# Kernel tuning notes

Hardware: AMD Instinct MI355X
Metric: run time of the kernel (lower is better)

Reference implementation:

```python
import jax, jax.numpy as jnp
import numpy as np

# 5x5 Gaussian-Laplacian template: kernel = (4*GL) * GL_T, with a2=-a1/8, a3=-a1/16
GL_T = np.zeros((5, 5), np.float32)
GL_T[2, 2] = 1.0
for r, c in [(1, 2), (2, 1), (2, 3), (3, 2)]:
    GL_T[r, c] = -1.0 / 8.0
for r, c in [(0, 2), (1, 1), (1, 3), (2, 0), (2, 4), (3, 1), (3, 3), (4, 2)]:
    GL_T[r, c] = -1.0 / 16.0

SOB0 = np.array([[1, 2, 1], [0, 0, 0], [-1, -2, -1]], np.float32)
SOB45 = np.array([[2, 1, 0], [1, 0, -1], [0, -1, -2]], np.float32)
SOB90 = np.array([[1, 0, -1], [2, 0, -2], [1, 0, -1]], np.float32)
SOB135 = np.array([[0, -1, -2], [1, 0, -1], [2, 1, 0]], np.float32)

# cubic-spaced threshold value table: (10-0)*(i/100)^3, i=0..100
X_VALUES = np.array([10.0 * (i / 100.0) ** 3 for i in range(101)], np.float32)


def conv2d(x, w, stride=1, padding=0):
    return jax.lax.conv_general_dilated(
        x, w, (stride, stride), ((padding, padding), (padding, padding)),
        dimension_numbers=("NCHW", "OIHW", "NCHW"))


def avg_pool(x, k, s, p):
    # PyTorch AvgPool2d default count_include_pad=True -> divide by k*k always
    s_ = jax.lax.reduce_window(x, 0.0, jax.lax.add, (1, 1, k, k), (1, 1, s, s),
                               ((0, 0), (0, 0), (p, p), (p, p)))
    return s_ / float(k * k)


def _gdm(x, gdm_weight, conv_w, bn_gamma, bn_beta, bn_mean, bn_var):
    x = avg_pool(x, 3, 2, 1)                                  # [B,3,H/2,W/2]
    image_a = jnp.mean(x, axis=1, keepdims=True)              # [B,1,h,w]
    y = conv2d(x, conv_w, stride=2, padding=3)                # ConvBN(3,5,7,s2)
    y = (y - bn_mean[None, :, None, None]) * jax.lax.rsqrt(bn_var + 1e-5)[None, :, None, None]
    y = y * bn_gamma[None, :, None, None] + bn_beta[None, :, None, None]
    weight_att = jnp.tanh(jnp.mean(y, axis=(2, 3)))           # [B,5]

    a1 = gdm_weight[0, 0] * 4.0
    kgl = (a1 * jnp.asarray(GL_T))[None, None]                # [1,1,5,5]
    x_GL = jnp.abs(conv2d(image_a, kgl, stride=1, padding=2))
    x_GL = jnp.where(x_GL < 1e-6, 0.0, x_GL)                  # abs/threshold; relu is no-op

    b, _, h, w = x_GL.shape
    x_t = x_GL.reshape(b, 1, -1)                              # [B,1,HW]
    x_max = jnp.max(x_t, axis=-1)                             # [B,1]
    pos = x_t > 0
    all_sum = jnp.sum(pos, axis=-1)                           # [B,1]
    xv = jnp.asarray(X_VALUES)[None, :, None]                 # [1,101,1]
    sub_sum = jnp.sum(pos & (x_t <= xv), axis=-1)             # [B,101]
    percentage = sub_sum / all_sum                            # [B,101] float

    params = jnp.stack([0.2 + 0.05 * weight_att[:, 1],
                        0.4 + 0.05 * weight_att[:, 2],
                        0.6 + 0.05 * weight_att[:, 3],
                        0.8 + 0.05 * weight_att[:, 4]])       # [4,B]
    thr_pct = jnp.sort(params, axis=0).T                      # [B,4]
    z = jnp.abs(percentage[:, None, :] - thr_pct[:, :, None]) # [B,4,101]
    closest = jnp.argmin(z, axis=-1)                          # [B,4]
    threshold = jnp.asarray(X_VALUES)[closest]                # [B,4]

    tmin = jnp.concatenate([jnp.zeros_like(x_max), threshold], axis=-1)[:, :, None]  # [B,5,1]
    tmax = jnp.concatenate([threshold, x_max], axis=-1)[:, :, None]                  # [B,5,1]
    mask = ((x_t > tmin) & (x_t <= tmax)).astype(jnp.float32)                        # [B,5,HW]
    m = mask.reshape(b, 5, h, w)

    m = avg_pool(m, 9, 1, 4)
    m = avg_pool(m, 9, 1, 4)
    m = avg_pool(m, 9, 2, 4)                                  # [B,5,h/2,w/2]
    mf = m.reshape(b, 5, -1)
    mn = jnp.min(mf, axis=2, keepdims=True)
    mx = jnp.max(mf, axis=2, keepdims=True)
    return ((mf - mn) / (mx - mn)).reshape(b, 5, h // 2, w // 2)


def _hge(feat, hge_weight, fc_w, fc_b):
    # directional kernels built from entries of the learned 3x3 weight
    Sob0 = hge_weight[:, :, 0, 0][:, :, None, None]
    Sob45 = hge_weight[:, :, 0, 1][:, :, None, None]
    Sob90 = hge_weight[:, :, 0, 2][:, :, None, None]
    Sob135 = hge_weight[:, :, 1, 0][:, :, None, None]
    a1 = (hge_weight[:, :, 2, 2] * 4.0)[:, :, None, None]
    x_0 = conv2d(feat, Sob0 * jnp.asarray(SOB0), 1, 1)
    x_45 = conv2d(feat, Sob45 * jnp.asarray(SOB45), 1, 1)
    x_90 = conv2d(feat, Sob90 * jnp.asarray(SOB90), 1, 1)
    x_135 = conv2d(feat, Sob135 * jnp.asarray(SOB135), 1, 1)
    x_GL = conv2d(feat, a1 * jnp.asarray(GL_T), 1, 2)
    x_out = jnp.concatenate([x_0, x_45, x_90, x_135, x_GL], axis=1)  # [B,5*C,H,W]
    return conv2d(x_out, fc_w) + fc_b[None, :, None, None]


def setup_inputs() -> dict:
    key = jax.random.key(0)
    ks = jax.random.split(key, 6)
    return {
        "x": jax.random.normal(ks[0], (8, 3, 512, 512), jnp.float32),
        "gdm_weight": jax.random.normal(ks[1], (1, 5), jnp.float32) * 0.5,
        "conv_w": jax.random.normal(ks[2], (5, 3, 7, 7), jnp.float32) * 0.05,
        "bn_gamma": jnp.ones((5,), jnp.float32),
        "bn_beta": jnp.zeros((5,), jnp.float32),
        "bn_mean": jnp.zeros((5,), jnp.float32),
        "bn_var": jnp.ones((5,), jnp.float32),
        "feat": jax.random.normal(ks[3], (8, 64, 128, 128), jnp.float32),
        "hge_weight": jax.random.normal(ks[4], (64, 64, 3, 3), jnp.float32) * 0.05,
        "fc_w": jax.random.normal(ks[5], (64, 320, 1, 1), jnp.float32) * 0.05,
        "fc_b": jnp.zeros((64,), jnp.float32),
    }


def reference(x, gdm_weight, conv_w, bn_gamma, bn_beta, bn_mean, bn_var,
              feat, hge_weight, fc_w, fc_b):
    gdm_out = _gdm(x, gdm_weight, conv_w, bn_gamma, bn_beta, bn_mean, bn_var)
    hge_out = _hge(feat, hge_weight, fc_w, fc_b)
    return gdm_out, hge_out
```

## Files before the change

### kernel.cpp

```cpp
#include <hip/hip_runtime.h>
#include <hip/hip_bf16.h>
#include <math.h>

#define WS_AT    0
#define WS_YSUM  20480
#define WS_XMAX  20520
#define WS_HIST  20528
#define WS_THR   21344
#define WS_MN    21376
#define WS_MX    21440
#define WS_XP    21504
#define WS_IA    1594368
#define WS_XGL   2118656

#define GDM_OUT  655360

static __device__ __forceinline__ float xv_val(int i) {
    double t = (double)i / 100.0;
    return (float)(10.0 * t * t * t);
}

__global__ __launch_bounds__(256) void k_front(const float* __restrict__ x,
                                               const float* __restrict__ hw,
                                               const float* __restrict__ fcw,
                                               float* __restrict__ xp,
                                               float* __restrict__ ia,
                                               float* __restrict__ At,
                                               float* __restrict__ zr) {
    int bid = blockIdx.x;
    if (bid < 2048) {
        int idx = bid * 256 + threadIdx.x;
        int b = idx >> 16; int p = idx & 65535; int oy = p >> 8; int ox = p & 255;
        float cs[3];
#pragma unroll
        for (int c = 0; c < 3; ++c) {
            const float* src = x + (((size_t)(b * 3 + c)) << 18);
            float s = 0.f;
#pragma unroll
            for (int dy = -1; dy <= 1; ++dy) {
                int iy = 2 * oy + dy; if ((unsigned)iy >= 512u) continue;
#pragma unroll
                for (int dx = -1; dx <= 1; ++dx) {
                    int ix = 2 * ox + dx; if ((unsigned)ix >= 512u) continue;
                    s += src[iy * 512 + ix];
                }
            }
            cs[c] = s * (1.f / 9.f);
            xp[(((size_t)(b * 3 + c)) << 16) + p] = cs[c];
        }
        ia[(((size_t)b) << 16) + p] = (cs[0] + cs[1] + cs[2]) * (1.f / 3.f);
    } else if (bid < 2128) {
        int idx = (bid - 2048) * 256 + threadIdx.x;
        int o = idx & 63; int k = idx >> 6;
        int d = k >> 6; int c = k & 63;
        const int goff[5] = {0, 1, 2, 3, 8};
        float s = 0.f;
        for (int m = 0; m < 64; ++m)
            s += fcw[o * 320 + d * 64 + m] * hw[(m * 64 + c) * 9 + goff[d]];
        At[k * 64 + o] = s * ((d == 4) ? 4.f : 1.f);
    } else {
#pragma unroll
        for (int q = 0; q < 4; ++q) {
            int i = threadIdx.x + 256 * q;
            if (i < 864) zr[i] = 0.f;
        }
    }
}

__global__ __launch_bounds__(256) void k_conv7(const float* __restrict__ xp,
                                               const float* __restrict__ w,
                                               float* __restrict__ ysum) {
    int b = blockIdx.y;
    int p = blockIdx.x * 256 + threadIdx.x;
    int oy = p >> 7, ox = p & 127;
    __shared__ float wsm[735];
    for (int l = threadIdx.x; l < 735; l += 256) wsm[l] = w[l];
    __syncthreads();
    float s[5] = {0.f, 0.f, 0.f, 0.f, 0.f};
    for (int ic = 0; ic < 3; ++ic) {
        const float* src = xp + (((size_t)(b * 3 + ic)) << 16);
#pragma unroll
        for (int r = 0; r < 7; ++r) {
            int iy = 2 * oy - 3 + r; if ((unsigned)iy >= 256u) continue;
#pragma unroll
            for (int ss = 0; ss < 7; ++ss) {
                int ix = 2 * ox - 3 + ss; if ((unsigned)ix >= 256u) continue;
                float v = src[iy * 256 + ix];
                int wi = (ic * 7 + r) * 7 + ss;
#pragma unroll
                for (int co = 0; co < 5; ++co) s[co] = fmaf(wsm[co * 147 + wi], v, s[co]);
            }
        }
    }
    __shared__ float red[256];
#pragma unroll
    for (int co = 0; co < 5; ++co) {
        red[threadIdx.x] = s[co]; __syncthreads();
        for (int off = 128; off > 0; off >>= 1) {
            if (threadIdx.x < off) red[threadIdx.x] += red[threadIdx.x + off];
            __syncthreads();
        }
        if (threadIdx.x == 0) atomicAdd(&ysum[b * 5 + co], red[0]);
        __syncthreads();
    }
}

__global__ __launch_bounds__(256) void k_gl_hist(const float* __restrict__ ia,
                                                 const float* __restrict__ gdmw,
                                                 float* __restrict__ xgl,
                                                 int* __restrict__ hist,
                                                 unsigned* __restrict__ xmax) {
    int b = blockIdx.y;
    int p = blockIdx.x * 256 + threadIdx.x;
    int y = p >> 8, x = p & 255;
    __shared__ float xv[101];
    __shared__ int sh[102];
    __shared__ float redm[256];
    if (threadIdx.x < 101) xv[threadIdx.x] = xv_val(threadIdx.x);
    if (threadIdx.x < 102) sh[threadIdx.x] = 0;
    __syncthreads();
    const float* src = ia + (((size_t)b) << 16);
    float a1 = gdmw[0] * 4.f;
    auto rd = [&](int dy, int dx) -> float {
        int iy = y + dy, ix = x + dx;
        if ((unsigned)iy >= 256u || (unsigned)ix >= 256u) return 0.f;
        return src[iy * 256 + ix];
    };
    float acc = rd(0, 0)
        - 0.125f  * (rd(-1, 0) + rd(0, -1) + rd(0, 1) + rd(1, 0))
        - 0.0625f * (rd(-2, 0) + rd(-1, -1) + rd(-1, 1) + rd(0, -2) +
                     rd(0, 2) + rd(1, -1) + rd(1, 1) + rd(2, 0));
    float raw = fabsf(a1 * acc);
    float val = (raw < 1e-6f) ? 0.f : raw;
    xgl[(((size_t)b) << 16) + p] = val;
    if (val > 0.f) {
        int lo = 0, hi = 101;
        while (lo < hi) { int mid = (lo + hi) >> 1; if (val <= xv[mid]) hi = mid; else lo = mid + 1; }
        atomicAdd(&sh[lo], 1);
    }
    redm[threadIdx.x] = val; __syncthreads();
    for (int off = 128; off > 0; off >>= 1) {
        if (threadIdx.x < off) redm[threadIdx.x] = fmaxf(redm[threadIdx.x], redm[threadIdx.x + off]);
        __syncthreads();
    }
    if (threadIdx.x == 0) atomicMax(&xmax[b], __float_as_uint(redm[0]));
    if (threadIdx.x < 102 && sh[threadIdx.x]) atomicAdd(&hist[b * 102 + threadIdx.x], sh[threadIdx.x]);
}

__global__ void k_thresholds(const float* __restrict__ ysum, const float* __restrict__ gamma,
                             const float* __restrict__ beta, const float* __restrict__ mean,
                             const float* __restrict__ var, const int* __restrict__ hist,
                             float* __restrict__ thr, unsigned* __restrict__ mnb,
                             unsigned* __restrict__ mxb) {
    int b = threadIdx.x;
    if (b >= 8) {
        if (b < 48) { mnb[b - 8] = 0x7f7fffffu; mxb[b - 8] = 0u; }
        return;
    }
    float wa[5];
    for (int c = 1; c < 5; ++c) {
        float m = ysum[b * 5 + c] * (1.f / 16384.f);
        wa[c] = tanhf((m - mean[c]) * rsqrtf(var[c] + 1e-5f) * gamma[c] + beta[c]);
    }
    float pr[4] = {0.2f + 0.05f * wa[1], 0.4f + 0.05f * wa[2],
                   0.6f + 0.05f * wa[3], 0.8f + 0.05f * wa[4]};
    auto sw = [&](int i, int j) { if (pr[i] > pr[j]) { float t = pr[i]; pr[i] = pr[j]; pr[j] = t; } };
    sw(0, 1); sw(2, 3); sw(0, 2); sw(1, 3); sw(1, 2);
    int all = 0;
    for (int i = 0; i <= 101; ++i) all += hist[b * 102 + i];
    float bestz[4] = {1e30f, 1e30f, 1e30f, 1e30f};
    int besti[4] = {0, 0, 0, 0};
    int cum = 0;
    for (int i = 0; i <= 100; ++i) {
        cum += hist[b * 102 + i];
        float pct = (float)cum / (float)all;
        for (int t = 0; t < 4; ++t) {
            float z = fabsf(pct - pr[t]);
            if (z < bestz[t]) { bestz[t] = z; besti[t] = i; }
        }
    }
    for (int t = 0; t < 4; ++t) thr[b * 4 + t] = xv_val(besti[t]);
}

#define F1_STR 268
__global__ __launch_bounds__(256) void k_hv1(const float* __restrict__ in,
                                             const float* __restrict__ thr,
                                             const unsigned* __restrict__ xmax,
                                             float* __restrict__ outp) {
    int plane = blockIdx.y;
    int r0 = blockIdx.x * 8;
    int b = plane / 5, band = plane - 5 * b;
    float tmin = (band == 0) ? 0.f : thr[b * 4 + band - 1];
    float tmax = (band == 4) ? __uint_as_float(xmax[b]) : thr[b * 4 + band];
    const float* src = in + (((size_t)b) << 16);
    __shared__ float mr[16][F1_STR];
    __shared__ float hh[16][256];
    int tid = threadIdx.x;
    for (int l = tid; l < 16 * 256; l += 256) {
        int i = l >> 8, c = l & 255;
        int rr = r0 - 4 + i;
        float v = ((unsigned)rr < 256u) ? src[rr * 256 + c] : 0.f;
        v = (v > tmin && v <= tmax) ? 1.f : 0.f;
        mr[i][c + 4] = v;
    }
    if (tid < 128) { int i = tid >> 3, p = tid & 7; mr[i][p < 4 ? p : 256 + p] = 0.f; }
    __syncthreads();
    {
        int r = tid >> 4, x0 = (tid & 15) * 16;
        float w[24];
#pragma unroll
        for (int k = 0; k < 6; ++k) {
            float4 q = *(const float4*)&mr[r][x0 + 4 * k];
            w[4 * k] = q.x; w[4 * k + 1] = q.y; w[4 * k + 2] = q.z; w[4 * k + 3] = q.w;
        }
        float o[16];
        float s = 0.f;
#pragma unroll
        for (int k = 0; k < 9; ++k) s += w[k];
#pragma unroll
        for (int j = 0; j < 16; ++j) {
            o[j] = s * (1.f / 9.f);
            if (j < 15) s += w[j + 9] - w[j];
        }
#pragma unroll
        for (int k = 0; k < 4; ++k) {
            float4 q = {o[4 * k], o[4 * k + 1], o[4 * k + 2], o[4 * k + 3]};
            *(float4*)&hh[r][x0 + 4 * k] = q;
        }
    }
    __syncthreads();
    {
        int c = tid;
        float ld[16];
#pragma unroll
        for (int i = 0; i < 16; ++i) ld[i] = hh[i][c];
        float s = 0.f;
#pragma unroll
        for (int k = 0; k < 9; ++k) s += ld[k];
        float* dst = outp + (((size_t)plane) << 16);
#pragma unroll
        for (int j = 0; j < 8; ++j) {
            dst[(r0 + j) * 256 + c] = s * (1.f / 9.f);
            if (j < 7) s += ld[j + 9] - ld[j];
        }
    }
}

__global__ __launch_bounds__(256) void k_hv2s2(const float* __restrict__ in,
                                               float* __restrict__ outp,
                                               unsigned* __restrict__ mnb,
                                               unsigned* __restrict__ mxb) {
    int plane = blockIdx.y;
    int r0 = blockIdx.x * 8;
    __shared__ float mr[31][264];
    __shared__ float hh[31][256];
    int tid = threadIdx.x;
    const float* src = in + (((size_t)plane) << 16);
    for (int l = tid; l < 31 * 264; l += 256) {
        int i = l / 264, c = l - i * 264;
        int rr = 2 * r0 - 8 + i, cc = c - 4;
        mr[i][c] = ((unsigned)rr < 256u && (unsigned)cc < 256u) ? src[rr * 256 + cc] : 0.f;
    }
    __syncthreads();
    for (int l = tid; l < 31 * 256; l += 256) {
        int i = l >> 8, x = l & 255;
        float s = 0.f;
#pragma unroll
        for (int k = 0; k < 9; ++k) s += mr[i][x + k];
        hh[i][x] = s * (1.f / 9.f);
    }
    __syncthreads();
    for (int l = tid; l < 23 * 256; l += 256) {
        int i2 = l >> 8, x = l & 255;
        float s = 0.f;
#pragma unroll
        for (int k = 0; k < 9; ++k) s += hh[i2 + k][x];
        float v = s * (1.f / 9.f);
        if ((unsigned)(2 * r0 - 4 + i2) >= 256u) v = 0.f;
        mr[i2][x + 4] = v;
    }
    if (tid < 184) { int i2 = tid / 8, p = tid & 7; mr[i2][p < 4 ? p : 256 + p] = 0.f; }
    __syncthreads();
    for (int l = tid; l < 23 * 128; l += 256) {
        int i2 = l >> 7, ox = l & 127;
        float s = 0.f;
#pragma unroll
        for (int k = 0; k < 9; ++k) s += mr[i2][2 * ox + k];
        hh[i2][ox] = s * (1.f / 9.f);
    }
    __syncthreads();
    float vmn = 1e30f, vmx = -1e30f;
    float* dst = outp + (size_t)plane * 16384;
#pragma unroll
    for (int q = 0; q < 4; ++q) {
        int l = tid + 256 * q;
        int jj = l >> 7, ox = l & 127;
        float s = 0.f;
#pragma unroll
        for (int k = 0; k < 9; ++k) s += hh[2 * jj + k][ox];
        s *= (1.f / 9.f);
        dst[(r0 + jj) * 128 + ox] = s;
        vmn = fminf(vmn, s); vmx = fmaxf(vmx, s);
    }
    __syncthreads();
    float* smn = &hh[23][0];
    float* smx = &hh[24][0];
    smn[tid] = vmn; smx[tid] = vmx; __syncthreads();
    for (int off = 128; off > 0; off >>= 1) {
        if (tid < off) {
            smn[tid] = fminf(smn[tid], smn[tid + off]);
            smx[tid] = fmaxf(smx[tid], smx[tid + off]);
        }
        __syncthreads();
    }
    if (tid == 0) {
        atomicMin(&mnb[plane], __float_as_uint(smn[0]));
        atomicMax(&mxb[plane], __float_as_uint(smx[0]));
    }
}

__global__ __launch_bounds__(256) void k_norm(const float* __restrict__ in,
                                              const unsigned* __restrict__ mnb,
                                              const unsigned* __restrict__ mxb,
                                              float* __restrict__ gdm) {
    int i4 = blockIdx.x * 256 + threadIdx.x;
    int idx = i4 * 4;
    int plane = idx >> 14;
    float mn = __uint_as_float(mnb[plane]), mx = __uint_as_float(mxb[plane]);
    float inv = 1.f / (mx - mn);
    float4 v = *(const float4*)&in[idx];
    float4 o = {(v.x - mn) * inv, (v.y - mn) * inv, (v.z - mn) * inv, (v.w - mn) * inv};
    *(float4*)&gdm[idx] = o;
}

__global__ __launch_bounds__(512, 2) void k_hge(const float* __restrict__ feat,
                                                const float* __restrict__ At,
                                                const float* __restrict__ fcb,
                                                float* __restrict__ out) {
    int tile = blockIdx.x, b = blockIdx.y;
    int ty = (tile >> 3) * 16, tx = (tile & 7) * 16;
    int tid = threadIdx.x;
    int grp = tid >> 8, tg = tid & 255;
    __shared__ float ft[2][20][21];
    __shared__ float tl[2][5][256];
    __shared__ float al[2][2][5][64];
    int og = tg >> 5, pg = tg & 31;
    float acc[8][4];
#pragma unroll
    for (int i = 0; i < 8; ++i)
#pragma unroll
        for (int j = 0; j < 4; ++j) acc[i][j] = 0.f;

    const float* cur[3];
    int str[3];
    bool ok[3];
#pragma unroll
    for (int j = 0; j < 3; ++j) {
        int l = tid + 512 * j;
        cur[j] = nullptr; str[j] = 0; ok[j] = false;
        if (l < 800) {
            int ch = (l >= 400); int rem = l - ch * 400;
            int r = rem / 20, cx = rem - r * 20;
            int gy = ty - 2 + r, gx = tx - 2 + cx;
            if ((unsigned)gy < 128u && (unsigned)gx < 128u) {
                cur[j] = feat + (((size_t)(b * 64 + ch)) << 14) + gy * 128 + gx;
                str[j] = 2 << 14;
                ok[j] = true;
            }
        } else if (l < 1440) {
            int q = l - 800;
            int ch = (q >= 320); int k = q - ch * 320;
            cur[j] = At + (k >> 6) * 4096 + ch * 64 + (k & 63);
            str[j] = 128;
            ok[j] = true;
        }
    }
    float pr[3];
#pragma unroll
    for (int j = 0; j < 3; ++j) pr[j] = ok[j] ? *cur[j] : 0.f;

    for (int g = 0; g < 32; ++g) {
        int buf = g & 1;
#pragma unroll
        for (int j = 0; j < 3; ++j) {
            int l = tid + 512 * j;
            if (l < 800) {
                int ch = (l >= 400); int rem = l - ch * 400;
                int r = rem / 20, cx = rem - r * 20;
                ft[ch][r][cx] = pr[j];
            } else if (l < 1440) {
                ((float*)al[buf])[l - 800] = pr[j];
            }
        }
        __syncthreads();
        if (g < 31) {
#pragma unroll
            for (int j = 0; j < 3; ++j) {
                if (ok[j]) { cur[j] += str[j]; pr[j] = *cur[j]; }
            }
        }
        {
            int cy = (tg >> 4) + 2, cx = (tg & 15) + 2;
            int ch = grp;
            float fm2 = ft[ch][cy - 2][cx], f2p = ft[ch][cy + 2][cx];
            float fl2 = ft[ch][cy][cx - 2], fr2 = ft[ch][cy][cx + 2];
            float a  = ft[ch][cy - 1][cx - 1], bq = ft[ch][cy - 1][cx], cc = ft[ch][cy - 1][cx + 1];
            float dd = ft[ch][cy][cx - 1],     ee = ft[ch][cy][cx],     ffv = ft[ch][cy][cx + 1];
            float g_ = ft[ch][cy + 1][cx - 1], h  = ft[ch][cy + 1][cx], i2 = ft[ch][cy + 1][cx + 1];
            tl[ch][0][tg] = (a + 2.f * bq + cc) - (g_ + 2.f * h + i2);
            tl[ch][1][tg] = 2.f * a + bq + dd - ffv - h - 2.f * i2;
            tl[ch][2][tg] = (a - cc) + 2.f * (dd - ffv) + (g_ - i2);
            tl[ch][3][tg] = -bq - 2.f * cc + dd - ffv + 2.f * g_ + h;
            tl[ch][4][tg] = ee - 0.125f * (bq + dd + ffv + h)
                          - 0.0625f * (fm2 + a + cc + fl2 + fr2 + g_ + i2 + f2p);
        }
        __syncthreads();
#pragma unroll
        for (int ch = 0; ch < 2; ++ch) {
#pragma unroll
            for (int d = 0; d < 5; ++d) {
                float4 a0 = *(const float4*)&al[buf][ch][d][grp * 32 + og * 4];
                float av[4] = {a0.x, a0.y, a0.z, a0.w};
#pragma unroll
                for (int pj = 0; pj < 8; ++pj) {
                    float tv = tl[ch][d][pg + 32 * pj];
#pragma unroll
                    for (int oi = 0; oi < 4; ++oi)
                        acc[pj][oi] = fmaf(av[oi], tv, acc[pj][oi]);
                }
            }
        }
    }
#pragma unroll
    for (int oi = 0; oi < 4; ++oi) {
        int o = grp * 32 + og * 4 + oi;
        float bias = fcb[o];
        float* dsto = out + (((size_t)(b * 64 + o)) << 14);
#pragma unroll
        for (int pj = 0; pj < 8; ++pj) {
            int pxl = pg + 32 * pj;
            dsto[(ty + (pxl >> 4)) * 128 + tx + (pxl & 15)] = acc[pj][oi] + bias;
        }
    }
}

extern "C" void kernel_launch(void* const* d_in, const int* in_sizes, int n_in,
                              void* d_out, int out_size, void* d_ws, size_t ws_size,
                              hipStream_t stream) {
    const float* x    = (const float*)d_in[0];
    const float* gdmw = (const float*)d_in[1];
    const float* convw= (const float*)d_in[2];
    const float* bng  = (const float*)d_in[3];
    const float* bnb  = (const float*)d_in[4];
    const float* bnm  = (const float*)d_in[5];
    const float* bnv  = (const float*)d_in[6];
    const float* feat = (const float*)d_in[7];
    const float* hw   = (const float*)d_in[8];
    const float* fcw  = (const float*)d_in[9];
    const float* fcb  = (const float*)d_in[10];
    float* out = (float*)d_out;
    float* ws  = (float*)d_ws;

    float* At   = ws + WS_AT;
    float* ysum = ws + WS_YSUM;
    unsigned* xmax = (unsigned*)(ws + WS_XMAX);
    int* hist   = (int*)(ws + WS_HIST);
    float* thr  = ws + WS_THR;
    unsigned* mnb = (unsigned*)(ws + WS_MN);
    unsigned* mxb = (unsigned*)(ws + WS_MX);
    float* xp   = ws + WS_XP;
    float* ia   = ws + WS_IA;
    float* xgl  = ws + WS_XGL;
    float* p2   = ws + WS_XP + 20480;

    float* hge = out + GDM_OUT;
    float* p0  = hge;

    k_front      <<<2129, 256, 0, stream>>>(x, hw, fcw, xp, ia, At, ws + WS_YSUM);
    k_conv7      <<<dim3(64, 8), 256, 0, stream>>>(xp, convw, ysum);
    k_gl_hist    <<<dim3(256, 8), 256, 0, stream>>>(ia, gdmw, xgl, hist, xmax);
    k_thresholds <<<1, 64, 0, stream>>>(ysum, bng, bnb, bnm, bnv, hist, thr, mnb, mxb);
    k_hv1        <<<dim3(32, 40), 256, 0, stream>>>(xgl, thr, xmax, p0);
    k_hv2s2      <<<dim3(16, 40), 256, 0, stream>>>(p0, p2, mnb, mxb);
    k_norm       <<<640, 256, 0, stream>>>(p2, mnb, mxb, out);
    k_hge        <<<dim3(64, 8), 512, 0, stream>>>(feat, At, fcb, hge);
}
```

Measured before the change: 250.4 us.

## Merge small kernels and process four channels per HGE iteration

```diff
diff --git a/kernel.cpp b/kernel.cpp
--- a/kernel.cpp
+++ b/kernel.cpp
@@ -26,7 +26,9 @@
                                                float* __restrict__ xp,
                                                float* __restrict__ ia,
                                                float* __restrict__ At,
-                                               float* __restrict__ zr) {
+                                               float* __restrict__ zr,
+                                               unsigned* __restrict__ mnb,
+                                               unsigned* __restrict__ mxb) {
     int bid = blockIdx.x;
     if (bid < 2048) {
         int idx = bid * 256 + threadIdx.x;
@@ -64,138 +66,140 @@
             int i = threadIdx.x + 256 * q;
             if (i < 864) zr[i] = 0.f;
         }
-    }
-}
-
-__global__ __launch_bounds__(256) void k_conv7(const float* __restrict__ xp,
-                                               const float* __restrict__ w,
-                                               float* __restrict__ ysum) {
-    int b = blockIdx.y;
-    int p = blockIdx.x * 256 + threadIdx.x;
-    int oy = p >> 7, ox = p & 127;
+        if (threadIdx.x < 40) mnb[threadIdx.x] = 0x7f7fffffu;
+        else if (threadIdx.x < 80) mxb[threadIdx.x - 40] = 0u;
+    }
+}
+
+__global__ __launch_bounds__(256) void k_convgl(const float* __restrict__ xp,
+                                                const float* __restrict__ w,
+                                                float* __restrict__ ysum,
+                                                const float* __restrict__ ia,
+                                                const float* __restrict__ gdmw,
+                                                float* __restrict__ xgl,
+                                                int* __restrict__ hist,
+                                                unsigned* __restrict__ xmax) {
     __shared__ float wsm[735];
-    for (int l = threadIdx.x; l < 735; l += 256) wsm[l] = w[l];
-    __syncthreads();
-    float s[5] = {0.f, 0.f, 0.f, 0.f, 0.f};
-    for (int ic = 0; ic < 3; ++ic) {
-        const float* src = xp + (((size_t)(b * 3 + ic)) << 16);
-#pragma unroll
-        for (int r = 0; r < 7; ++r) {
-            int iy = 2 * oy - 3 + r; if ((unsigned)iy >= 256u) continue;
-#pragma unroll
-            for (int ss = 0; ss < 7; ++ss) {
-                int ix = 2 * ox - 3 + ss; if ((unsigned)ix >= 256u) continue;
-                float v = src[iy * 256 + ix];
-                int wi = (ic * 7 + r) * 7 + ss;
-#pragma unroll
-                for (int co = 0; co < 5; ++co) s[co] = fmaf(wsm[co * 147 + wi], v, s[co]);
-            }
-        }
-    }
     __shared__ float red[256];
-#pragma unroll
-    for (int co = 0; co < 5; ++co) {
-        red[threadIdx.x] = s[co]; __syncthreads();
-        for (int off = 128; off > 0; off >>= 1) {
-            if (threadIdx.x < off) red[threadIdx.x] += red[threadIdx.x + off];
-            __syncthreads();
-        }
-        if (threadIdx.x == 0) atomicAdd(&ysum[b * 5 + co], red[0]);
-        __syncthreads();
-    }
-}
-
-__global__ __launch_bounds__(256) void k_gl_hist(const float* __restrict__ ia,
-                                                 const float* __restrict__ gdmw,
-                                                 float* __restrict__ xgl,
-                                                 int* __restrict__ hist,
-                                                 unsigned* __restrict__ xmax) {
-    int b = blockIdx.y;
-    int p = blockIdx.x * 256 + threadIdx.x;
-    int y = p >> 8, x = p & 255;
     __shared__ float xv[101];
     __shared__ int sh[102];
-    __shared__ float redm[256];
-    if (threadIdx.x < 101) xv[threadIdx.x] = xv_val(threadIdx.x);
-    if (threadIdx.x < 102) sh[threadIdx.x] = 0;
-    __syncthreads();
-    const float* src = ia + (((size_t)b) << 16);
-    float a1 = gdmw[0] * 4.f;
-    auto rd = [&](int dy, int dx) -> float {
-        int iy = y + dy, ix = x + dx;
-        if ((unsigned)iy >= 256u || (unsigned)ix >= 256u) return 0.f;
-        return src[iy * 256 + ix];
-    };
-    float acc = rd(0, 0)
-        - 0.125f  * (rd(-1, 0) + rd(0, -1) + rd(0, 1) + rd(1, 0))
-        - 0.0625f * (rd(-2, 0) + rd(-1, -1) + rd(-1, 1) + rd(0, -2) +
-                     rd(0, 2) + rd(1, -1) + rd(1, 1) + rd(2, 0));
-    float raw = fabsf(a1 * acc);
-    float val = (raw < 1e-6f) ? 0.f : raw;
-    xgl[(((size_t)b) << 16) + p] = val;
-    if (val > 0.f) {
-        int lo = 0, hi = 101;
-        while (lo < hi) { int mid = (lo + hi) >> 1; if (val <= xv[mid]) hi = mid; else lo = mid + 1; }
-        atomicAdd(&sh[lo], 1);
-    }
-    redm[threadIdx.x] = val; __syncthreads();
-    for (int off = 128; off > 0; off >>= 1) {
-        if (threadIdx.x < off) redm[threadIdx.x] = fmaxf(redm[threadIdx.x], redm[threadIdx.x + off]);
+    int bid = blockIdx.x;
+    int tid = threadIdx.x;
+    if (bid < 512) {
+        int b = bid >> 6;
+        int p = (bid & 63) * 256 + tid;
+        int oy = p >> 7, ox = p & 127;
+        for (int l = tid; l < 735; l += 256) wsm[l] = w[l];
         __syncthreads();
-    }
-    if (threadIdx.x == 0) atomicMax(&xmax[b], __float_as_uint(redm[0]));
-    if (threadIdx.x < 102 && sh[threadIdx.x]) atomicAdd(&hist[b * 102 + threadIdx.x], sh[threadIdx.x]);
-}
-
-__global__ void k_thresholds(const float* __restrict__ ysum, const float* __restrict__ gamma,
-                             const float* __restrict__ beta, const float* __restrict__ mean,
-                             const float* __restrict__ var, const int* __restrict__ hist,
-                             float* __restrict__ thr, unsigned* __restrict__ mnb,
-                             unsigned* __restrict__ mxb) {
-    int b = threadIdx.x;
-    if (b >= 8) {
-        if (b < 48) { mnb[b - 8] = 0x7f7fffffu; mxb[b - 8] = 0u; }
-        return;
-    }
-    float wa[5];
-    for (int c = 1; c < 5; ++c) {
-        float m = ysum[b * 5 + c] * (1.f / 16384.f);
-        wa[c] = tanhf((m - mean[c]) * rsqrtf(var[c] + 1e-5f) * gamma[c] + beta[c]);
-    }
-    float pr[4] = {0.2f + 0.05f * wa[1], 0.4f + 0.05f * wa[2],
-                   0.6f + 0.05f * wa[3], 0.8f + 0.05f * wa[4]};
-    auto sw = [&](int i, int j) { if (pr[i] > pr[j]) { float t = pr[i]; pr[i] = pr[j]; pr[j] = t; } };
-    sw(0, 1); sw(2, 3); sw(0, 2); sw(1, 3); sw(1, 2);
-    int all = 0;
-    for (int i = 0; i <= 101; ++i) all += hist[b * 102 + i];
-    float bestz[4] = {1e30f, 1e30f, 1e30f, 1e30f};
-    int besti[4] = {0, 0, 0, 0};
-    int cum = 0;
-    for (int i = 0; i <= 100; ++i) {
-        cum += hist[b * 102 + i];
-        float pct = (float)cum / (float)all;
-        for (int t = 0; t < 4; ++t) {
-            float z = fabsf(pct - pr[t]);
-            if (z < bestz[t]) { bestz[t] = z; besti[t] = i; }
-        }
-    }
-    for (int t = 0; t < 4; ++t) thr[b * 4 + t] = xv_val(besti[t]);
+        float s[5] = {0.f, 0.f, 0.f, 0.f, 0.f};
+        for (int ic = 0; ic < 3; ++ic) {
+            const float* src = xp + (((size_t)(b * 3 + ic)) << 16);
+#pragma unroll
+            for (int r = 0; r < 7; ++r) {
+                int iy = 2 * oy - 3 + r; if ((unsigned)iy >= 256u) continue;
+#pragma unroll
+                for (int ss = 0; ss < 7; ++ss) {
+                    int ix = 2 * ox - 3 + ss; if ((unsigned)ix >= 256u) continue;
+                    float v = src[iy * 256 + ix];
+                    int wi = (ic * 7 + r) * 7 + ss;
+#pragma unroll
+                    for (int co = 0; co < 5; ++co) s[co] = fmaf(wsm[co * 147 + wi], v, s[co]);
+                }
+            }
+        }
+#pragma unroll
+        for (int co = 0; co < 5; ++co) {
+            red[tid] = s[co]; __syncthreads();
+            for (int off = 128; off > 0; off >>= 1) {
+                if (tid < off) red[tid] += red[tid + off];
+                __syncthreads();
+            }
+            if (tid == 0) atomicAdd(&ysum[b * 5 + co], red[0]);
+            __syncthreads();
+        }
+    } else {
+        int idx = bid - 512;
+        int b = idx >> 8;
+        int p = (idx & 255) * 256 + tid;
+        int y = p >> 8, x = p & 255;
+        if (tid < 101) xv[tid] = xv_val(tid);
+        if (tid < 102) sh[tid] = 0;
+        __syncthreads();
+        const float* src = ia + (((size_t)b) << 16);
+        float a1 = gdmw[0] * 4.f;
+        auto rd = [&](int dy, int dx) -> float {
+            int iy = y + dy, ix = x + dx;
+            if ((unsigned)iy >= 256u || (unsigned)ix >= 256u) return 0.f;
+            return src[iy * 256 + ix];
+        };
+        float acc = rd(0, 0)
+            - 0.125f  * (rd(-1, 0) + rd(0, -1) + rd(0, 1) + rd(1, 0))
+            - 0.0625f * (rd(-2, 0) + rd(-1, -1) + rd(-1, 1) + rd(0, -2) +
+                         rd(0, 2) + rd(1, -1) + rd(1, 1) + rd(2, 0));
+        float raw = fabsf(a1 * acc);
+        float val = (raw < 1e-6f) ? 0.f : raw;
+        xgl[(((size_t)b) << 16) + p] = val;
+        if (val > 0.f) {
+            int lo = 0, hi = 101;
+            while (lo < hi) { int mid = (lo + hi) >> 1; if (val <= xv[mid]) hi = mid; else lo = mid + 1; }
+            atomicAdd(&sh[lo], 1);
+        }
+        red[tid] = val; __syncthreads();
+        for (int off = 128; off > 0; off >>= 1) {
+            if (tid < off) red[tid] = fmaxf(red[tid], red[tid + off]);
+            __syncthreads();
+        }
+        if (tid == 0) atomicMax(&xmax[b], __float_as_uint(red[0]));
+        if (tid < 102 && sh[tid]) atomicAdd(&hist[b * 102 + tid], sh[tid]);
+    }
 }
 
 #define F1_STR 268
 __global__ __launch_bounds__(256) void k_hv1(const float* __restrict__ in,
-                                             const float* __restrict__ thr,
+                                             const float* __restrict__ ysum,
+                                             const float* __restrict__ gamma,
+                                             const float* __restrict__ beta,
+                                             const float* __restrict__ mean,
+                                             const float* __restrict__ var,
+                                             const int* __restrict__ hist,
                                              const unsigned* __restrict__ xmax,
                                              float* __restrict__ outp) {
     int plane = blockIdx.y;
     int r0 = blockIdx.x * 8;
     int b = plane / 5, band = plane - 5 * b;
-    float tmin = (band == 0) ? 0.f : thr[b * 4 + band - 1];
-    float tmax = (band == 4) ? __uint_as_float(xmax[b]) : thr[b * 4 + band];
+    __shared__ float sthr[4];
+    int tid = threadIdx.x;
+    if (tid == 0) {
+        float wa[5];
+        for (int c = 1; c < 5; ++c) {
+            float m = ysum[b * 5 + c] * (1.f / 16384.f);
+            wa[c] = tanhf((m - mean[c]) * rsqrtf(var[c] + 1e-5f) * gamma[c] + beta[c]);
+        }
+        float pr[4] = {0.2f + 0.05f * wa[1], 0.4f + 0.05f * wa[2],
+                       0.6f + 0.05f * wa[3], 0.8f + 0.05f * wa[4]};
+        auto sw = [&](int i, int j) { if (pr[i] > pr[j]) { float t = pr[i]; pr[i] = pr[j]; pr[j] = t; } };
+        sw(0, 1); sw(2, 3); sw(0, 2); sw(1, 3); sw(1, 2);
+        int all = 0;
+        for (int i = 0; i <= 101; ++i) all += hist[b * 102 + i];
+        float bestz[4] = {1e30f, 1e30f, 1e30f, 1e30f};
+        int besti[4] = {0, 0, 0, 0};
+        int cum = 0;
+        for (int i = 0; i <= 100; ++i) {
+            cum += hist[b * 102 + i];
+            float pct = (float)cum / (float)all;
+            for (int t = 0; t < 4; ++t) {
+                float z = fabsf(pct - pr[t]);
+                if (z < bestz[t]) { bestz[t] = z; besti[t] = i; }
+            }
+        }
+        for (int t = 0; t < 4; ++t) sthr[t] = xv_val(besti[t]);
+    }
+    __syncthreads();
+    float tmin = (band == 0) ? 0.f : sthr[band - 1];
+    float tmax = (band == 4) ? __uint_as_float(xmax[b]) : sthr[band];
     const float* src = in + (((size_t)b) << 16);
     __shared__ float mr[16][F1_STR];
     __shared__ float hh[16][256];
-    int tid = threadIdx.x;
     for (int l = tid; l < 16 * 256; l += 256) {
         int i = l >> 8, c = l & 255;
         int rr = r0 - 4 + i;
@@ -319,31 +323,36 @@
     }
 }
 
-__global__ __launch_bounds__(256) void k_norm(const float* __restrict__ in,
-                                              const unsigned* __restrict__ mnb,
-                                              const unsigned* __restrict__ mxb,
-                                              float* __restrict__ gdm) {
-    int i4 = blockIdx.x * 256 + threadIdx.x;
-    int idx = i4 * 4;
-    int plane = idx >> 14;
-    float mn = __uint_as_float(mnb[plane]), mx = __uint_as_float(mxb[plane]);
-    float inv = 1.f / (mx - mn);
-    float4 v = *(const float4*)&in[idx];
-    float4 o = {(v.x - mn) * inv, (v.y - mn) * inv, (v.z - mn) * inv, (v.w - mn) * inv};
-    *(float4*)&gdm[idx] = o;
-}
-
 __global__ __launch_bounds__(512, 2) void k_hge(const float* __restrict__ feat,
                                                 const float* __restrict__ At,
                                                 const float* __restrict__ fcb,
+                                                const float* __restrict__ p2,
+                                                const unsigned* __restrict__ mnb,
+                                                const unsigned* __restrict__ mxb,
+                                                float* __restrict__ gdm,
                                                 float* __restrict__ out) {
     int tile = blockIdx.x, b = blockIdx.y;
+    int tid = threadIdx.x;
+    if (tile == 64) {
+        int base = b * 512 + tid;
+#pragma unroll
+        for (int q = 0; q < 40; ++q) {
+            int i4 = base + 4096 * q;
+            int idx = i4 * 4;
+            int plane = idx >> 14;
+            float mn = __uint_as_float(mnb[plane]), mx = __uint_as_float(mxb[plane]);
+            float inv = 1.f / (mx - mn);
+            float4 v = *(const float4*)&p2[idx];
+            float4 o = {(v.x - mn) * inv, (v.y - mn) * inv, (v.z - mn) * inv, (v.w - mn) * inv};
+            *(float4*)&gdm[idx] = o;
+        }
+        return;
+    }
     int ty = (tile >> 3) * 16, tx = (tile & 7) * 16;
-    int tid = threadIdx.x;
     int grp = tid >> 8, tg = tid & 255;
-    __shared__ float ft[2][20][21];
-    __shared__ float tl[2][5][256];
-    __shared__ float al[2][2][5][64];
+    __shared__ float ft[4][20][21];
+    __shared__ float tl[4][5][256];
+    __shared__ float al[2][4][5][64];
     int og = tg >> 5, pg = tg & 31;
     float acc[8][4];
 #pragma unroll
@@ -351,72 +360,75 @@
 #pragma unroll
         for (int j = 0; j < 4; ++j) acc[i][j] = 0.f;
 
-    const float* cur[3];
-    int str[3];
-    bool ok[3];
-#pragma unroll
-    for (int j = 0; j < 3; ++j) {
+    const float* cur[6];
+    int str6[6], lof[6], typ[6];
+    bool ok[6];
+#pragma unroll
+    for (int j = 0; j < 6; ++j) {
         int l = tid + 512 * j;
-        cur[j] = nullptr; str[j] = 0; ok[j] = false;
-        if (l < 800) {
-            int ch = (l >= 400); int rem = l - ch * 400;
+        cur[j] = nullptr; str6[j] = 0; lof[j] = 0; typ[j] = 2; ok[j] = false;
+        if (l < 1600) {
+            int ch = l / 400, rem = l - ch * 400;
             int r = rem / 20, cx = rem - r * 20;
+            lof[j] = ch * 420 + r * 21 + cx;
+            typ[j] = 0;
             int gy = ty - 2 + r, gx = tx - 2 + cx;
             if ((unsigned)gy < 128u && (unsigned)gx < 128u) {
                 cur[j] = feat + (((size_t)(b * 64 + ch)) << 14) + gy * 128 + gx;
-                str[j] = 2 << 14;
+                str6[j] = 4 << 14;
                 ok[j] = true;
             }
-        } else if (l < 1440) {
-            int q = l - 800;
-            int ch = (q >= 320); int k = q - ch * 320;
+        } else if (l < 2880) {
+            int q = l - 1600;
+            int ch = q / 320, k = q - ch * 320;
             cur[j] = At + (k >> 6) * 4096 + ch * 64 + (k & 63);
-            str[j] = 128;
+            str6[j] = 256;
+            lof[j] = ch * 320 + k;
+            typ[j] = 1;
             ok[j] = true;
         }
     }
-    float pr[3];
-#pragma unroll
-    for (int j = 0; j < 3; ++j) pr[j] = ok[j] ? *cur[j] : 0.f;
-
-    for (int g = 0; g < 32; ++g) {
+    float pf[6];
+#pragma unroll
+    for (int j = 0; j < 6; ++j) pf[j] = ok[j] ? *cur[j] : 0.f;
+
+    float* ftb = &ft[0][0][0];
+    for (int g = 0; g < 16; ++g) {
         int buf = g & 1;
-#pragma unroll
-        for (int j = 0; j < 3; ++j) {
-            int l = tid + 512 * j;
-            if (l < 800) {
-                int ch = (l >= 400); int rem = l - ch * 400;
-                int r = rem / 20, cx = rem - r * 20;
-                ft[ch][r][cx] = pr[j];
-            } else if (l < 1440) {
-                ((float*)al[buf])[l - 800] = pr[j];
-            }
+        float* alb = (float*)al[buf];
+#pragma unroll
+        for (int j = 0; j < 6; ++j) {
+            if (typ[j] == 0) ftb[lof[j]] = pf[j];
+            else if (typ[j] == 1) alb[lof[j]] = pf[j];
         }
         __syncthreads();
-        if (g < 31) {
-#pragma unroll
-            for (int j = 0; j < 3; ++j) {
-                if (ok[j]) { cur[j] += str[j]; pr[j] = *cur[j]; }
-            }
-        }
-        {
-            int cy = (tg >> 4) + 2, cx = (tg & 15) + 2;
-            int ch = grp;
-            float fm2 = ft[ch][cy - 2][cx], f2p = ft[ch][cy + 2][cx];
-            float fl2 = ft[ch][cy][cx - 2], fr2 = ft[ch][cy][cx + 2];
-            float a  = ft[ch][cy - 1][cx - 1], bq = ft[ch][cy - 1][cx], cc = ft[ch][cy - 1][cx + 1];
-            float dd = ft[ch][cy][cx - 1],     ee = ft[ch][cy][cx],     ffv = ft[ch][cy][cx + 1];
-            float g_ = ft[ch][cy + 1][cx - 1], h  = ft[ch][cy + 1][cx], i2 = ft[ch][cy + 1][cx + 1];
-            tl[ch][0][tg] = (a + 2.f * bq + cc) - (g_ + 2.f * h + i2);
-            tl[ch][1][tg] = 2.f * a + bq + dd - ffv - h - 2.f * i2;
-            tl[ch][2][tg] = (a - cc) + 2.f * (dd - ffv) + (g_ - i2);
-            tl[ch][3][tg] = -bq - 2.f * cc + dd - ffv + 2.f * g_ + h;
-            tl[ch][4][tg] = ee - 0.125f * (bq + dd + ffv + h)
+        if (g < 15) {
+#pragma unroll
+            for (int j = 0; j < 6; ++j) {
+                if (ok[j]) { cur[j] += str6[j]; pf[j] = *cur[j]; }
+            }
+        }
+#pragma unroll
+        for (int q = 0; q < 2; ++q) {
+            int item = tid + 512 * q;
+            int px = item & 255, ch = item >> 8;
+            int cy = (px >> 4) + 2, cx = (px & 15) + 2;
+            const float (*F)[21] = ft[ch];
+            float fm2 = F[cy - 2][cx], f2p = F[cy + 2][cx];
+            float fl2 = F[cy][cx - 2], fr2 = F[cy][cx + 2];
+            float a  = F[cy - 1][cx - 1], bq = F[cy - 1][cx], cc = F[cy - 1][cx + 1];
+            float dd = F[cy][cx - 1],     ee = F[cy][cx],     ffv = F[cy][cx + 1];
+            float g_ = F[cy + 1][cx - 1], h  = F[cy + 1][cx], i2 = F[cy + 1][cx + 1];
+            tl[ch][0][px] = (a + 2.f * bq + cc) - (g_ + 2.f * h + i2);
+            tl[ch][1][px] = 2.f * a + bq + dd - ffv - h - 2.f * i2;
+            tl[ch][2][px] = (a - cc) + 2.f * (dd - ffv) + (g_ - i2);
+            tl[ch][3][px] = -bq - 2.f * cc + dd - ffv + 2.f * g_ + h;
+            tl[ch][4][px] = ee - 0.125f * (bq + dd + ffv + h)
                           - 0.0625f * (fm2 + a + cc + fl2 + fr2 + g_ + i2 + f2p);
         }
         __syncthreads();
 #pragma unroll
-        for (int ch = 0; ch < 2; ++ch) {
+        for (int ch = 0; ch < 4; ++ch) {
 #pragma unroll
             for (int d = 0; d < 5; ++d) {
                 float4 a0 = *(const float4*)&al[buf][ch][d][grp * 32 + og * 4];
@@ -465,7 +477,6 @@
     float* ysum = ws + WS_YSUM;
     unsigned* xmax = (unsigned*)(ws + WS_XMAX);
     int* hist   = (int*)(ws + WS_HIST);
-    float* thr  = ws + WS_THR;
     unsigned* mnb = (unsigned*)(ws + WS_MN);
     unsigned* mxb = (unsigned*)(ws + WS_MX);
     float* xp   = ws + WS_XP;
@@ -476,12 +487,9 @@
     float* hge = out + GDM_OUT;
     float* p0  = hge;
 
-    k_front      <<<2129, 256, 0, stream>>>(x, hw, fcw, xp, ia, At, ws + WS_YSUM);
-    k_conv7      <<<dim3(64, 8), 256, 0, stream>>>(xp, convw, ysum);
-    k_gl_hist    <<<dim3(256, 8), 256, 0, stream>>>(ia, gdmw, xgl, hist, xmax);
-    k_thresholds <<<1, 64, 0, stream>>>(ysum, bng, bnb, bnm, bnv, hist, thr, mnb, mxb);
-    k_hv1        <<<dim3(32, 40), 256, 0, stream>>>(xgl, thr, xmax, p0);
-    k_hv2s2      <<<dim3(16, 40), 256, 0, stream>>>(p0, p2, mnb, mxb);
-    k_norm       <<<640, 256, 0, stream>>>(p2, mnb, mxb, out);
-    k_hge        <<<dim3(64, 8), 512, 0, stream>>>(feat, At, fcb, hge);
-}
+    k_front  <<<2129, 256, 0, stream>>>(x, hw, fcw, xp, ia, At, ws + WS_YSUM, mnb, mxb);
+    k_convgl <<<2560, 256, 0, stream>>>(xp, convw, ysum, ia, gdmw, xgl, hist, xmax);
+    k_hv1    <<<dim3(32, 40), 256, 0, stream>>>(xgl, ysum, bng, bnb, bnm, bnv, hist, xmax, p0);
+    k_hv2s2  <<<dim3(16, 40), 256, 0, stream>>>(p0, p2, mnb, mxb);
+    k_hge    <<<dim3(65, 8), 512, 0, stream>>>(feat, At, fcb, p2, mnb, mxb, out, hge);
+}
```

New measurement: 305.2 us. 1.22x slower.
